# Kernel optimization log

Measured on AMD Instinct MI355X. Metric: run time of the kernel, lower is better.

Reference implementation:

```python
import jax, jax.numpy as jnp
import numpy as np

EPS = 1e-5

def _conv(x, w, b, dil, pad, groups):
    y = jax.lax.conv_general_dilated(
        x, w, window_strides=(1, 1), padding=[(pad, pad), (pad, pad)],
        rhs_dilation=(dil, dil), dimension_numbers=('NCHW', 'OIHW', 'NCHW'),
        feature_group_count=groups)
    return y + b[None, :, None, None]

def setup_inputs() -> dict:
    key = jax.random.key(0)
    ks = jax.random.split(key, 12)
    B, C, H, W = 16, 128, 128, 128
    half = C // 2  # 64
    x = jax.random.normal(ks[0], (B, C, H, W), dtype=jnp.float32)
    # depthwise 3x3 (groups=half) + pointwise 1x1
    dw_w = jax.random.normal(ks[1], (half, 1, 3, 3), dtype=jnp.float32) * 0.1
    dw_b = jax.random.normal(ks[2], (half,), dtype=jnp.float32) * 0.1
    pw_w = jax.random.normal(ks[3], (half, half, 1, 1), dtype=jnp.float32) * (1.0 / np.sqrt(half))
    pw_b = jax.random.normal(ks[4], (half,), dtype=jnp.float32) * 0.1
    # four 1->1 channel 3x3 convs with dilations 1..4 (weights shared across blocks)
    mcc_w = jax.random.normal(ks[5], (4, 1, 1, 3, 3), dtype=jnp.float32) * 0.2
    mcc_b = jax.random.normal(ks[6], (4,), dtype=jnp.float32) * 0.1
    gamma = jnp.ones((C,), dtype=jnp.float32)
    beta = jnp.zeros((C,), dtype=jnp.float32)
    return {"x": x, "dw_w": dw_w, "dw_b": dw_b, "pw_w": pw_w, "pw_b": pw_b,
            "mcc_w": mcc_w, "mcc_b": mcc_b, "gamma": gamma, "beta": beta}

def reference(x, dw_w, dw_b, pw_w, pw_b, mcc_w, mcc_b, gamma, beta):
    B, C, H, W = x.shape
    half = C // 2
    nblk = half // 4
    # split_channel: even channels -> x1, odd channels -> x2
    x1 = x[:, 0::2]
    x2 = x[:, 1::2]
    # branch 1: depthwise 3x3 then pointwise 1x1
    x1 = _conv(x1, dw_w, dw_b, dil=1, pad=1, groups=half)
    x1 = _conv(x1, pw_w, pw_b, dil=1, pad=0, groups=1)
    # branch 2: channel i of x2 goes through dilated conv (i mod 4); vectorize by
    # gathering channels j::4 and running one depthwise conv per dilation.
    ys = []
    for j in range(4):
        d = j + 1
        xj = x2[:, j::4]                       # [B, nblk, H, W]
        wj = jnp.tile(mcc_w[j], (nblk, 1, 1, 1))  # [nblk,1,3,3] shared kernel
        bj = jnp.tile(mcc_b[j], (nblk,))
        ys.append(_conv(xj, wj, bj, dil=d, pad=d, groups=nblk))
    # interleave back: channel 4*b+j <- ys[j][:, b]
    mcc = jnp.stack(ys, axis=2).reshape(B, half, H, W)
    fusion = jnp.concatenate([x1, mcc], axis=1)  # [B, C, H, W]
    # BatchNorm2d (training mode: batch statistics, biased variance) + ReLU
    mean = jnp.mean(fusion, axis=(0, 2, 3), keepdims=True)
    var = jnp.var(fusion, axis=(0, 2, 3), keepdims=True)
    norm = (fusion - mean) * jax.lax.rsqrt(var + EPS)
    out = norm * gamma[None, :, None, None] + beta[None, :, None, None]
    return jax.nn.relu(out)
```

## Files before the change

kernel.cpp:

```cpp
#include <hip/hip_runtime.h>
#include <hip/hip_bf16.h>

#define Bn 16
#define Cn 128
#define Hn 128
#define Wn 128
#define HWn (Hn*Wn)
#define CHWn (Cn*HWn)
#define HALF 64
#define NTOT (Bn*HWn)
#define NSLOT 32
#define NITEM 10240

#define DT_P 76
#define CB_P 136
#define SMEM_BYTES 22528

typedef __attribute__((ext_vector_type(8))) short short8;
typedef __attribute__((ext_vector_type(4))) float floatx4;
typedef float __attribute__((ext_vector_type(4))) f32x4;

__device__ __forceinline__ float4 fma4(float s, float4 v, float4 a) {
  a.x = fmaf(s, v.x, a.x); a.y = fmaf(s, v.y, a.y);
  a.z = fmaf(s, v.z, a.z); a.w = fmaf(s, v.w, a.w);
  return a;
}
__device__ __forceinline__ unsigned short f2bf(float f) {
  union { __hip_bfloat16 h; unsigned short u; } cv;
  cv.h = __float2bfloat16(f); return cv.u;
}
__device__ __forceinline__ float bf2f(unsigned short u) {
  union { unsigned short u; __hip_bfloat16 h; } cv; cv.u = u;
  return __bfloat162float(cv.h);
}
__device__ __forceinline__ unsigned pk2f(float a, float b) {
  return (unsigned)f2bf(a) | ((unsigned)f2bf(b) << 16);
}
__device__ __forceinline__ short8 ld_frag(const unsigned short* p) {
  union { uint2 u[2]; short8 s; } cv;
  cv.u[0] = *(const uint2*)p;
  cv.u[1] = *(const uint2*)(p + 4);
  return cv.s;
}
__device__ __forceinline__ void st_nt4(float* p, float4 v) {
  f32x4 w = {v.x, v.y, v.z, v.w};
  __builtin_nontemporal_store(w, (f32x4*)p);
}

__device__ __forceinline__ float4 row3(float4 acc, float4 B, float wa, float wb,
                                       float wc, int lane31) {
  float xl = __shfl_up(B.w, 1);
  float xr = __shfl_down(B.x, 1);
  if (lane31 == 0)  xl = 0.f;
  if (lane31 == 31) xr = 0.f;
  float4 L = make_float4(xl, B.x, B.y, B.z);
  float4 R = make_float4(B.y, B.z, B.w, xr);
  acc = fma4(wa, L, acc);
  acc = fma4(wb, B, acc);
  acc = fma4(wc, R, acc);
  return acc;
}

template<bool BF16>
__device__ __forceinline__ void dwpw_body(
    const int item, const int t, unsigned char* __restrict__ smem,
    const float* __restrict__ x, const float* __restrict__ pw_w,
    const float* __restrict__ dw_w, const float* __restrict__ dw_b,
    const float* __restrict__ pw_b, float* __restrict__ outf,
    __hip_bfloat16* __restrict__ outh, float* __restrict__ stats)
{
  unsigned short* DtCb = (unsigned short*)smem;
  float* dww  = (float*)(smem + 128*DT_P*2);
  float* sred = dww + 640;

  const int band = item & 7;
  const int ri   = item >> 3;
  const int h = band*16 + (ri & 15);
  const int b = ri >> 4;

  for (int i = t; i < 576; i += 256) {
    int k = i / 9, j = i - k*9;
    dww[j*64 + k] = dw_w[i];
  }
  if (t < 64)  dww[576 + t] = dw_b[t];
  if (t < 128) sred[t] = 0.f;
  __syncthreads();

  {
    const int lane31 = t & 31;
    const int px4 = lane31 << 2;
    const int k0 = t >> 5;
    const float* xb = x + (size_t)b*CHWn + (size_t)h*Wn + px4;
    const bool hasU = (h > 0), hasD = (h < Hn-1);
    const float4 z4 = make_float4(0.f,0.f,0.f,0.f);
    unsigned lo[4];
    #pragma unroll
    for (int i = 0; i < 8; ++i) {
      const int k = k0*8 + i;
      const float* xc = xb + (size_t)(2*k)*HWn;
      float4 r0 = hasU ? *(const float4*)(xc - Wn) : z4;
      float4 r1 = *(const float4*)xc;
      float4 r2 = hasD ? *(const float4*)(xc + Wn) : z4;
      float bk = dww[576 + k];
      float4 a = make_float4(bk, bk, bk, bk);
      a = row3(a, r0, dww[0*64+k], dww[1*64+k], dww[2*64+k], lane31);
      a = row3(a, r1, dww[3*64+k], dww[4*64+k], dww[5*64+k], lane31);
      a = row3(a, r2, dww[6*64+k], dww[7*64+k], dww[8*64+k], lane31);
      float av[4] = {a.x, a.y, a.z, a.w};
      if ((i & 1) == 0) {
        #pragma unroll
        for (int j = 0; j < 4; ++j) lo[j] = f2bf(av[j]);
      } else {
        #pragma unroll
        for (int j = 0; j < 4; ++j) {
          unsigned pk = lo[j] | ((unsigned)f2bf(av[j]) << 16);
          *(unsigned*)&DtCb[(px4+j)*DT_P + k0*8 + (i-1)] = pk;
        }
      }
    }
  }
  __syncthreads();

  const int lane = t & 63;
  const int wv   = t >> 6;
  const int q4   = lane >> 4;
  const int n16  = lane & 15;

  short8 Af[4][2], Bf[2][2];
  #pragma unroll
  for (int ct = 0; ct < 4; ++ct)
    #pragma unroll
    for (int kc = 0; kc < 2; ++kc) {
      const float* wp = pw_w + (ct*16 + n16)*64 + kc*32 + q4*8;
      float4 w0 = *(const float4*)wp;
      float4 w1 = *(const float4*)(wp + 4);
      union { unsigned u[4]; short8 s; } cv;
      cv.u[0] = pk2f(w0.x, w0.y); cv.u[1] = pk2f(w0.z, w0.w);
      cv.u[2] = pk2f(w1.x, w1.y); cv.u[3] = pk2f(w1.z, w1.w);
      Af[ct][kc] = cv.s;
    }
  #pragma unroll
  for (int nt = 0; nt < 2; ++nt)
    #pragma unroll
    for (int kc = 0; kc < 2; ++kc)
      Bf[nt][kc] = ld_frag(&DtCb[(wv*32 + nt*16 + n16)*DT_P + kc*32 + q4*8]);

  floatx4 C[4][2];
  #pragma unroll
  for (int ct = 0; ct < 4; ++ct) {
    float4 bs = *(const float4*)&pw_b[ct*16 + q4*4];
    floatx4 ini = {bs.x, bs.y, bs.z, bs.w};
    C[ct][0] = ini; C[ct][1] = ini;
  }
  #pragma unroll
  for (int kc = 0; kc < 2; ++kc)
    #pragma unroll
    for (int ct = 0; ct < 4; ++ct)
      #pragma unroll
      for (int nt = 0; nt < 2; ++nt)
        C[ct][nt] = __builtin_amdgcn_mfma_f32_16x16x32_bf16(
            Af[ct][kc], Bf[nt][kc], C[ct][nt], 0, 0, 0);

  __syncthreads();

  #pragma unroll
  for (int ct = 0; ct < 4; ++ct) {
    float S[4], Q[4];
    #pragma unroll
    for (int r = 0; r < 4; ++r) {
      float a = C[ct][0][r], c2 = C[ct][1][r];
      S[r] = a + c2;
      Q[r] = a*a + c2*c2;
    }
    #pragma unroll
    for (int off = 1; off < 16; off <<= 1)
      #pragma unroll
      for (int r = 0; r < 4; ++r) {
        S[r] += __shfl_xor(S[r], off);
        Q[r] += __shfl_xor(Q[r], off);
      }
    if (n16 == 0) {
      #pragma unroll
      for (int r = 0; r < 4; ++r) {
        int c = ct*16 + q4*4 + r;
        atomicAdd(&sred[c], S[r]);
        atomicAdd(&sred[64 + c], Q[r]);
      }
    }
  }

  const size_t ob = (size_t)b*CHWn + (size_t)h*Wn;
  if (BF16) {
    #pragma unroll
    for (int ct = 0; ct < 4; ++ct)
      #pragma unroll
      for (int nt = 0; nt < 2; ++nt)
        #pragma unroll
        for (int r = 0; r < 4; ++r) {
          int c  = ct*16 + q4*4 + r;
          int px = wv*32 + nt*16 + n16;
          DtCb[c*CB_P + px] = f2bf(C[ct][nt][r]);
        }
  } else {
    #pragma unroll
    for (int ct = 0; ct < 4; ++ct)
      #pragma unroll
      for (int nt = 0; nt < 2; ++nt)
        #pragma unroll
        for (int r = 0; r < 4; ++r) {
          int c  = ct*16 + q4*4 + r;
          int px = wv*32 + nt*16 + n16;
          outf[ob + (size_t)c*HWn + px] = C[ct][nt][r];
        }
  }
  __syncthreads();

  if (BF16) {
    for (int i = t; i < 1024; i += 256) {
      int c = i >> 4, p8 = (i & 15) << 3;
      uint4 v = *(const uint4*)&DtCb[c*CB_P + p8];
      *(uint4*)(outh + ob + (size_t)c*HWn + p8) = v;
    }
  }

  float* sg = stats + (item & (NSLOT-1))*256;
  if (t < 64)       atomicAdd(&sg[t], sred[t]);
  else if (t < 128) atomicAdd(&sg[64 + t], sred[t]);
}

template<int D> __device__ __forceinline__ float4 shiftL(float4 A, float4 B) {
  if (D == 1) return make_float4(A.w, B.x, B.y, B.z);
  if (D == 2) return make_float4(A.z, A.w, B.x, B.y);
  if (D == 3) return make_float4(A.y, A.z, A.w, B.x);
  return A;
}
template<int D> __device__ __forceinline__ float4 shiftR(float4 B, float4 C) {
  if (D == 1) return make_float4(B.y, B.z, B.w, C.x);
  if (D == 2) return make_float4(B.z, B.w, C.x, C.y);
  if (D == 3) return make_float4(B.w, C.x, C.y, C.z);
  return C;
}

template<bool BF16, int D>
__device__ __forceinline__ void mcc_compute(
    const float* __restrict__ xc, const float* __restrict__ wj, float bj,
    float* __restrict__ outf, __hip_bfloat16* __restrict__ outh,
    float* lds, int t, int h0, float& s, float& q)
{
  const int R = 16 + 2*D;
  for (int idx = t; idx < R*32; idx += 256) {
    int r = idx >> 5, p4 = (idx & 31) << 2;
    int gr = h0 - D + r;
    float4 v = make_float4(0.f,0.f,0.f,0.f);
    if (gr >= 0 && gr < Hn) v = *(const float4*)(xc + gr*Wn + p4);
    *(float4*)&lds[r*128 + p4] = v;
  }
  __syncthreads();
  const int px4 = (t & 31) << 2;
  const int rl  = t >> 5;
  s = 0.f; q = 0.f;
  #pragma unroll
  for (int rr = 0; rr < 2; ++rr) {
    const int row = rl + rr*8;
    float4 acc = make_float4(bj, bj, bj, bj);
    #pragma unroll
    for (int dr = 0; dr < 3; ++dr) {
      const float* lrow = &lds[(row + dr*D)*128];
      float4 B4 = *(const float4*)(lrow + px4);
      float4 A4 = make_float4(0.f,0.f,0.f,0.f);
      float4 C4 = make_float4(0.f,0.f,0.f,0.f);
      if (px4 > 0)   A4 = *(const float4*)(lrow + px4 - 4);
      if (px4 < 124) C4 = *(const float4*)(lrow + px4 + 4);
      acc = fma4(wj[dr*3+0], shiftL<D>(A4, B4), acc);
      acc = fma4(wj[dr*3+1], B4, acc);
      acc = fma4(wj[dr*3+2], shiftR<D>(B4, C4), acc);
    }
    if (BF16) {
      uint2 pk; pk.x = pk2f(acc.x, acc.y); pk.y = pk2f(acc.z, acc.w);
      *(uint2*)(outh + (size_t)(h0+row)*Wn + px4) = pk;
    } else {
      *(float4*)(outf + (size_t)(h0+row)*Wn + px4) = acc;
    }
    s += acc.x + acc.y + acc.z + acc.w;
    q += acc.x*acc.x + acc.y*acc.y + acc.z*acc.z + acc.w*acc.w;
  }
}

template<bool BF16>
__device__ __forceinline__ void mcc_body(
    const int mi, const int t, unsigned char* __restrict__ smem,
    const float* __restrict__ x, const float* __restrict__ mcc_w,
    const float* __restrict__ mcc_b, float* __restrict__ outf,
    __hip_bfloat16* __restrict__ outh, float* __restrict__ stats)
{
  float* lds = (float*)smem;
  float* red = lds + 24*128;

  const int hb = mi & 7;
  const int m  = (mi >> 3) & 63;
  const int b  = mi >> 9;
  const int j  = m & 3;
  const int h0 = hb << 4;

  const float* xc = x + (size_t)b*CHWn + (size_t)(2*m+1)*HWn;
  const size_t oo = (size_t)b*CHWn + (size_t)(HALF+m)*HWn;
  float* of = BF16 ? nullptr : outf + oo;
  __hip_bfloat16* oh = BF16 ? outh + oo : nullptr;
  const float* wj = mcc_w + j*9;
  const float bj = mcc_b[j];

  float s = 0.f, q = 0.f;
  switch (j) {
    case 0:  mcc_compute<BF16,1>(xc, wj, bj, of, oh, lds, t, h0, s, q); break;
    case 1:  mcc_compute<BF16,2>(xc, wj, bj, of, oh, lds, t, h0, s, q); break;
    case 2:  mcc_compute<BF16,3>(xc, wj, bj, of, oh, lds, t, h0, s, q); break;
    default: mcc_compute<BF16,4>(xc, wj, bj, of, oh, lds, t, h0, s, q); break;
  }

  #pragma unroll
  for (int off = 32; off > 0; off >>= 1) {
    s += __shfl_down(s, off);
    q += __shfl_down(q, off);
  }
  const int wvi = t >> 6;
  if ((t & 63) == 0) { red[wvi] = s; red[4+wvi] = q; }
  __syncthreads();
  if (t == 0) {
    float* sg = stats + (mi & (NSLOT-1))*256;
    atomicAdd(&sg[HALF + m],       red[0]+red[1]+red[2]+red[3]);
    atomicAdd(&sg[128 + HALF + m], red[4]+red[5]+red[6]+red[7]);
  }
}

template<bool BF16>
__global__ __launch_bounds__(256, 3) void fused_kernel(
    const float* __restrict__ x, const float* __restrict__ pw_w,
    const float* __restrict__ dw_w, const float* __restrict__ dw_b,
    const float* __restrict__ pw_b, const float* __restrict__ mcc_w,
    const float* __restrict__ mcc_b, float* __restrict__ outf,
    __hip_bfloat16* __restrict__ outh, float* __restrict__ stats)
{
  __shared__ __align__(16) unsigned char smem[SMEM_BYTES];
  const int bid = blockIdx.x;
  const int t = threadIdx.x;
  const int qt = bid / 5;
  if (bid - qt*5 == 0)
    dwpw_body<BF16>(qt, t, smem, x, pw_w, dw_w, dw_b, pw_b, outf, outh, stats);
  else
    mcc_body<BF16>(bid - qt - 1, t, smem, x, mcc_w, mcc_b, outf, outh, stats);
}

__global__ __launch_bounds__(64) void finalize_kernel(
    const float* __restrict__ stats, const float* __restrict__ gamma,
    const float* __restrict__ beta, float* __restrict__ scsh)
{
  const int c = blockIdx.x;
  const int t = threadIdx.x;
  int idx = (t < 32) ? c : (128 + c);
  float v = stats[(t & 31)*256 + idx];
  #pragma unroll
  for (int off = 1; off < 32; off <<= 1) v += __shfl_xor(v, off);
  float S = __shfl(v, 0);
  float Q = __shfl(v, 32);
  if (t == 0) {
    const float n = (float)NTOT;
    float mean = S / n;
    float var  = Q / n - mean*mean;
    float sc = gamma[c] / sqrtf(var + 1e-5f);
    scsh[2*c]   = sc;
    scsh[2*c+1] = beta[c] - mean*sc;
  }
}

__global__ __launch_bounds__(256) void norm_bf_kernel(
    const unsigned short* __restrict__ inh, float* __restrict__ out,
    const float* __restrict__ scsh)
{
  const int blk = blockIdx.x;
  const int plane = blk >> 2;
  const int quarter = blk & 3;
  const int c = plane & 127;
  const float sc = scsh[2*c], sh = scsh[2*c+1];
  const int t = threadIdx.x;

  const uint4* in = (const uint4*)(inh + (size_t)plane*HWn) + quarter*512;
  float* op = out + (size_t)plane*HWn + quarter*4096;
  uint4 p[2];
  #pragma unroll
  for (int i = 0; i < 2; ++i) p[i] = in[t + i*256];
  #pragma unroll
  for (int i = 0; i < 2; ++i) {
    int idx = t + i*256;
    float4 a, bq;
    a.x = fmaxf(fmaf(bf2f(p[i].x & 0xffff), sc, sh), 0.f);
    a.y = fmaxf(fmaf(bf2f(p[i].x >> 16),    sc, sh), 0.f);
    a.z = fmaxf(fmaf(bf2f(p[i].y & 0xffff), sc, sh), 0.f);
    a.w = fmaxf(fmaf(bf2f(p[i].y >> 16),    sc, sh), 0.f);
    bq.x = fmaxf(fmaf(bf2f(p[i].z & 0xffff), sc, sh), 0.f);
    bq.y = fmaxf(fmaf(bf2f(p[i].z >> 16),    sc, sh), 0.f);
    bq.z = fmaxf(fmaf(bf2f(p[i].w & 0xffff), sc, sh), 0.f);
    bq.w = fmaxf(fmaf(bf2f(p[i].w >> 16),    sc, sh), 0.f);
    st_nt4(op + idx*8,     a);
    st_nt4(op + idx*8 + 4, bq);
  }
}

__global__ __launch_bounds__(256) void norm_f32_kernel(float* __restrict__ out,
    const float* __restrict__ scsh)
{
  const int blk = blockIdx.x;
  const int plane = blk >> 2;
  const int quarter = blk & 3;
  const int c = plane & 127;
  const float sc = scsh[2*c], sh = scsh[2*c+1];
  float* op = out + (size_t)plane*HWn + quarter*4096;
  #pragma unroll
  for (int i = 0; i < 4; ++i) {
    int idx = threadIdx.x + i*256;
    float4 v = ((const float4*)op)[idx];
    v.x = fmaxf(fmaf(v.x, sc, sh), 0.f);
    v.y = fmaxf(fmaf(v.y, sc, sh), 0.f);
    v.z = fmaxf(fmaf(v.z, sc, sh), 0.f);
    v.w = fmaxf(fmaf(v.w, sc, sh), 0.f);
    ((float4*)op)[idx] = v;
  }
}

extern "C" void kernel_launch(void* const* d_in, const int* in_sizes, int n_in,
                              void* d_out, int out_size, void* d_ws, size_t ws_size,
                              hipStream_t stream)
{
  (void)in_sizes; (void)n_in; (void)out_size;
  const float* x     = (const float*)d_in[0];
  const float* dw_w  = (const float*)d_in[1];
  const float* dw_b  = (const float*)d_in[2];
  const float* pw_w  = (const float*)d_in[3];
  const float* pw_b  = (const float*)d_in[4];
  const float* mcc_w = (const float*)d_in[5];
  const float* mcc_b = (const float*)d_in[6];
  const float* gamma = (const float*)d_in[7];
  const float* beta  = (const float*)d_in[8];
  float* out   = (float*)d_out;
  float* stats = (float*)d_ws;
  float* scsh  = (float*)((char*)d_ws + 32768);
  __hip_bfloat16* bf = (__hip_bfloat16*)((char*)d_ws + 34816);
  const size_t need = 34816 + (size_t)Bn*CHWn*2;
  const bool useBF = ws_size >= need;

  hipMemsetAsync(d_ws, 0, 32768, stream);
  if (useBF) {
    fused_kernel<true><<<NITEM, 256, 0, stream>>>(x, pw_w, dw_w, dw_b, pw_b,
                                                  mcc_w, mcc_b, nullptr, bf, stats);
    finalize_kernel<<<Cn, 64, 0, stream>>>(stats, gamma, beta, scsh);
    norm_bf_kernel<<<Bn*Cn*4, 256, 0, stream>>>((const unsigned short*)bf, out, scsh);
  } else {
    fused_kernel<false><<<NITEM, 256, 0, stream>>>(x, pw_w, dw_w, dw_b, pw_b,
                                                   mcc_w, mcc_b, out, nullptr, stats);
    finalize_kernel<<<Cn, 64, 0, stream>>>(stats, gamma, beta, scsh);
    norm_f32_kernel<<<Bn*Cn*4, 256, 0, stream>>>(out, scsh);
  }
}
```

Baseline: 315.3 us.

## Enlarge dilated-conv row tiles, hoist depthwise loads, use plain output stores

The dilated-conv work items now cover 32 rows instead of 16, which halves the number of those blocks and cuts the relative halo reload overhead. The fused grid shrinks to match, keeping one depthwise/pointwise block per two dilated-conv blocks. In the depthwise stage, all 24 float4 input loads are issued up front to expose more memory-level parallelism. The final normalize kernel also switches from nontemporal stores to regular stores. The risks are higher register pressure under the 3-blocks-per-CU launch bound and fewer blocks available for load balancing.

```diff
diff --git a/kernel.cpp b/kernel.cpp
--- a/kernel.cpp
+++ b/kernel.cpp
@@ -10,7 +10,7 @@
 #define HALF 64
 #define NTOT (Bn*HWn)
 #define NSLOT 32
-#define NITEM 10240
+#define NBLK 6144
 
 #define DT_P 76
 #define CB_P 136
@@ -18,7 +18,6 @@
 
 typedef __attribute__((ext_vector_type(8))) short short8;
 typedef __attribute__((ext_vector_type(4))) float floatx4;
-typedef float __attribute__((ext_vector_type(4))) f32x4;
 
 __device__ __forceinline__ float4 fma4(float s, float4 v, float4 a) {
   a.x = fmaf(s, v.x, a.x); a.y = fmaf(s, v.y, a.y);
@@ -41,10 +40,6 @@
   cv.u[0] = *(const uint2*)p;
   cv.u[1] = *(const uint2*)(p + 4);
   return cv.s;
-}
-__device__ __forceinline__ void st_nt4(float* p, float4 v) {
-  f32x4 w = {v.x, v.y, v.z, v.w};
-  __builtin_nontemporal_store(w, (f32x4*)p);
 }
 
 __device__ __forceinline__ float4 row3(float4 acc, float4 B, float wa, float wb,
@@ -93,19 +88,25 @@
     const float* xb = x + (size_t)b*CHWn + (size_t)h*Wn + px4;
     const bool hasU = (h > 0), hasD = (h < Hn-1);
     const float4 z4 = make_float4(0.f,0.f,0.f,0.f);
+
+    float4 R0[8], R1[8], R2[8];
+    #pragma unroll
+    for (int i = 0; i < 8; ++i) {
+      const float* xc = xb + (size_t)(2*(k0*8 + i))*HWn;
+      R0[i] = hasU ? *(const float4*)(xc - Wn) : z4;
+      R1[i] = *(const float4*)xc;
+      R2[i] = hasD ? *(const float4*)(xc + Wn) : z4;
+    }
+
     unsigned lo[4];
     #pragma unroll
     for (int i = 0; i < 8; ++i) {
       const int k = k0*8 + i;
-      const float* xc = xb + (size_t)(2*k)*HWn;
-      float4 r0 = hasU ? *(const float4*)(xc - Wn) : z4;
-      float4 r1 = *(const float4*)xc;
-      float4 r2 = hasD ? *(const float4*)(xc + Wn) : z4;
       float bk = dww[576 + k];
       float4 a = make_float4(bk, bk, bk, bk);
-      a = row3(a, r0, dww[0*64+k], dww[1*64+k], dww[2*64+k], lane31);
-      a = row3(a, r1, dww[3*64+k], dww[4*64+k], dww[5*64+k], lane31);
-      a = row3(a, r2, dww[6*64+k], dww[7*64+k], dww[8*64+k], lane31);
+      a = row3(a, R0[i], dww[0*64+k], dww[1*64+k], dww[2*64+k], lane31);
+      a = row3(a, R1[i], dww[3*64+k], dww[4*64+k], dww[5*64+k], lane31);
+      a = row3(a, R2[i], dww[6*64+k], dww[7*64+k], dww[8*64+k], lane31);
       float av[4] = {a.x, a.y, a.z, a.w};
       if ((i & 1) == 0) {
         #pragma unroll
@@ -247,7 +248,7 @@
     float* __restrict__ outf, __hip_bfloat16* __restrict__ outh,
     float* lds, int t, int h0, float& s, float& q)
 {
-  const int R = 16 + 2*D;
+  const int R = 32 + 2*D;
   for (int idx = t; idx < R*32; idx += 256) {
     int r = idx >> 5, p4 = (idx & 31) << 2;
     int gr = h0 - D + r;
@@ -260,7 +261,7 @@
   const int rl  = t >> 5;
   s = 0.f; q = 0.f;
   #pragma unroll
-  for (int rr = 0; rr < 2; ++rr) {
+  for (int rr = 0; rr < 4; ++rr) {
     const int row = rl + rr*8;
     float4 acc = make_float4(bj, bj, bj, bj);
     #pragma unroll
@@ -294,13 +295,13 @@
     __hip_bfloat16* __restrict__ outh, float* __restrict__ stats)
 {
   float* lds = (float*)smem;
-  float* red = lds + 24*128;
-
-  const int hb = mi & 7;
-  const int m  = (mi >> 3) & 63;
-  const int b  = mi >> 9;
+  float* red = (float*)(smem + 40*128*4);
+
+  const int hb = mi & 3;
+  const int m  = (mi >> 2) & 63;
+  const int b  = mi >> 8;
   const int j  = m & 3;
-  const int h0 = hb << 4;
+  const int h0 = hb << 5;
 
   const float* xc = x + (size_t)b*CHWn + (size_t)(2*m+1)*HWn;
   const size_t oo = (size_t)b*CHWn + (size_t)(HALF+m)*HWn;
@@ -343,8 +344,8 @@
   __shared__ __align__(16) unsigned char smem[SMEM_BYTES];
   const int bid = blockIdx.x;
   const int t = threadIdx.x;
-  const int qt = bid / 5;
-  if (bid - qt*5 == 0)
+  const int qt = bid / 3;
+  if (bid - qt*3 == 0)
     dwpw_body<BF16>(qt, t, smem, x, pw_w, dw_w, dw_b, pw_b, outf, outh, stats);
   else
     mcc_body<BF16>(bid - qt - 1, t, smem, x, mcc_w, mcc_b, outf, outh, stats);
@@ -400,8 +401,8 @@
     bq.y = fmaxf(fmaf(bf2f(p[i].z >> 16),    sc, sh), 0.f);
     bq.z = fmaxf(fmaf(bf2f(p[i].w & 0xffff), sc, sh), 0.f);
     bq.w = fmaxf(fmaf(bf2f(p[i].w >> 16),    sc, sh), 0.f);
-    st_nt4(op + idx*8,     a);
-    st_nt4(op + idx*8 + 4, bq);
+    *(float4*)(op + idx*8)     = a;
+    *(float4*)(op + idx*8 + 4) = bq;
   }
 }
 
@@ -449,13 +450,13 @@
 
   hipMemsetAsync(d_ws, 0, 32768, stream);
   if (useBF) {
-    fused_kernel<true><<<NITEM, 256, 0, stream>>>(x, pw_w, dw_w, dw_b, pw_b,
-                                                  mcc_w, mcc_b, nullptr, bf, stats);
+    fused_kernel<true><<<NBLK, 256, 0, stream>>>(x, pw_w, dw_w, dw_b, pw_b,
+                                                 mcc_w, mcc_b, nullptr, bf, stats);
     finalize_kernel<<<Cn, 64, 0, stream>>>(stats, gamma, beta, scsh);
     norm_bf_kernel<<<Bn*Cn*4, 256, 0, stream>>>((const unsigned short*)bf, out, scsh);
   } else {
-    fused_kernel<false><<<NITEM, 256, 0, stream>>>(x, pw_w, dw_w, dw_b, pw_b,
-                                                   mcc_w, mcc_b, out, nullptr, stats);
+    fused_kernel<false><<<NBLK, 256, 0, stream>>>(x, pw_w, dw_w, dw_b, pw_b,
+                                                  mcc_w, mcc_b, out, nullptr, stats);
     finalize_kernel<<<Cn, 64, 0, stream>>>(stats, gamma, beta, scsh);
     norm_f32_kernel<<<Bn*Cn*4, 256, 0, stream>>>(out, scsh);
   }
```

Measured after the change: 321.9 us. +2.1%, slower.

## Merge conv, stats finalize and normalize into one cooperative persistent kernel

Applied to the files above, without the earlier changes.

Replaces the three-kernel sequence (fused conv with stats, finalize, normalize) with a single cooperative persistent kernel that loops over work items and separates the phases with grid-wide syncs. The aim is to remove two kernel launch gaps and tail effects between phases. The cost is a smaller persistent grid limited by occupancy, a grid-stride loop over 10240 items that may balance worse, and the overhead of grid barriers.

```diff
diff --git a/kernel.cpp b/kernel.cpp
--- a/kernel.cpp
+++ b/kernel.cpp
@@ -1,5 +1,8 @@
 #include <hip/hip_runtime.h>
 #include <hip/hip_bf16.h>
+#include <hip/hip_cooperative_groups.h>
+
+namespace cg = cooperative_groups;
 
 #define Bn 16
 #define Cn 128
@@ -332,56 +335,14 @@
   }
 }
 
-template<bool BF16>
-__global__ __launch_bounds__(256, 3) void fused_kernel(
-    const float* __restrict__ x, const float* __restrict__ pw_w,
-    const float* __restrict__ dw_w, const float* __restrict__ dw_b,
-    const float* __restrict__ pw_b, const float* __restrict__ mcc_w,
-    const float* __restrict__ mcc_b, float* __restrict__ outf,
-    __hip_bfloat16* __restrict__ outh, float* __restrict__ stats)
-{
-  __shared__ __align__(16) unsigned char smem[SMEM_BYTES];
-  const int bid = blockIdx.x;
-  const int t = threadIdx.x;
-  const int qt = bid / 5;
-  if (bid - qt*5 == 0)
-    dwpw_body<BF16>(qt, t, smem, x, pw_w, dw_w, dw_b, pw_b, outf, outh, stats);
-  else
-    mcc_body<BF16>(bid - qt - 1, t, smem, x, mcc_w, mcc_b, outf, outh, stats);
-}
-
-__global__ __launch_bounds__(64) void finalize_kernel(
-    const float* __restrict__ stats, const float* __restrict__ gamma,
-    const float* __restrict__ beta, float* __restrict__ scsh)
-{
-  const int c = blockIdx.x;
-  const int t = threadIdx.x;
-  int idx = (t < 32) ? c : (128 + c);
-  float v = stats[(t & 31)*256 + idx];
-  #pragma unroll
-  for (int off = 1; off < 32; off <<= 1) v += __shfl_xor(v, off);
-  float S = __shfl(v, 0);
-  float Q = __shfl(v, 32);
-  if (t == 0) {
-    const float n = (float)NTOT;
-    float mean = S / n;
-    float var  = Q / n - mean*mean;
-    float sc = gamma[c] / sqrtf(var + 1e-5f);
-    scsh[2*c]   = sc;
-    scsh[2*c+1] = beta[c] - mean*sc;
-  }
-}
-
-__global__ __launch_bounds__(256) void norm_bf_kernel(
+__device__ __forceinline__ void norm_quarter(
     const unsigned short* __restrict__ inh, float* __restrict__ out,
-    const float* __restrict__ scsh)
-{
-  const int blk = blockIdx.x;
+    const float* __restrict__ scsh, int blk, int t)
+{
   const int plane = blk >> 2;
   const int quarter = blk & 3;
   const int c = plane & 127;
   const float sc = scsh[2*c], sh = scsh[2*c+1];
-  const int t = threadIdx.x;
 
   const uint4* in = (const uint4*)(inh + (size_t)plane*HWn) + quarter*512;
   float* op = out + (size_t)plane*HWn + quarter*4096;
@@ -403,6 +364,96 @@
     st_nt4(op + idx*8,     a);
     st_nt4(op + idx*8 + 4, bq);
   }
+}
+
+__device__ __forceinline__ void finalize_one(
+    const float* __restrict__ stats, const float* __restrict__ gamma,
+    const float* __restrict__ beta, float* __restrict__ scsh, int c, int t)
+{
+  if (t < 64) {
+    int idx = (t < 32) ? c : (128 + c);
+    float v = stats[(t & 31)*256 + idx];
+    #pragma unroll
+    for (int off = 1; off < 32; off <<= 1) v += __shfl_xor(v, off);
+    float S = __shfl(v, 0);
+    float Q = __shfl(v, 32);
+    if (t == 0) {
+      const float n = (float)NTOT;
+      float mean = S / n;
+      float var  = Q / n - mean*mean;
+      float sc = gamma[c] / sqrtf(var + 1e-5f);
+      scsh[2*c]   = sc;
+      scsh[2*c+1] = beta[c] - mean*sc;
+    }
+  }
+}
+
+__global__ __launch_bounds__(256, 3) void mega_kernel(
+    const float* __restrict__ x, const float* __restrict__ pw_w,
+    const float* __restrict__ dw_w, const float* __restrict__ dw_b,
+    const float* __restrict__ pw_b, const float* __restrict__ mcc_w,
+    const float* __restrict__ mcc_b, const float* __restrict__ gamma,
+    const float* __restrict__ beta, __hip_bfloat16* __restrict__ bf,
+    float* __restrict__ stats, float* __restrict__ scsh,
+    float* __restrict__ out)
+{
+  __shared__ __align__(16) unsigned char smem[SMEM_BYTES];
+  cg::grid_group gg = cg::this_grid();
+  const int t = threadIdx.x;
+  const int G = gridDim.x;
+
+  for (int item = blockIdx.x; item < NITEM; item += G) {
+    __syncthreads();
+    const int q = item / 5;
+    if (item - q*5 == 0)
+      dwpw_body<true>(q, t, smem, x, pw_w, dw_w, dw_b, pw_b,
+                      nullptr, bf, stats);
+    else
+      mcc_body<true>(item - q - 1, t, smem, x, mcc_w, mcc_b,
+                     nullptr, bf, stats);
+  }
+  __threadfence();
+  gg.sync();
+
+  for (int c = blockIdx.x; c < Cn; c += G)
+    finalize_one(stats, gamma, beta, scsh, c, t);
+  __threadfence();
+  gg.sync();
+
+  for (int hp = blockIdx.x; hp < Bn*Cn*4; hp += G)
+    norm_quarter((const unsigned short*)bf, out, scsh, hp, t);
+}
+
+template<bool BF16>
+__global__ __launch_bounds__(256, 3) void fused_kernel(
+    const float* __restrict__ x, const float* __restrict__ pw_w,
+    const float* __restrict__ dw_w, const float* __restrict__ dw_b,
+    const float* __restrict__ pw_b, const float* __restrict__ mcc_w,
+    const float* __restrict__ mcc_b, float* __restrict__ outf,
+    __hip_bfloat16* __restrict__ outh, float* __restrict__ stats)
+{
+  __shared__ __align__(16) unsigned char smem[SMEM_BYTES];
+  const int bid = blockIdx.x;
+  const int t = threadIdx.x;
+  const int qt = bid / 5;
+  if (bid - qt*5 == 0)
+    dwpw_body<BF16>(qt, t, smem, x, pw_w, dw_w, dw_b, pw_b, outf, outh, stats);
+  else
+    mcc_body<BF16>(bid - qt - 1, t, smem, x, mcc_w, mcc_b, outf, outh, stats);
+}
+
+__global__ __launch_bounds__(64) void finalize_kernel(
+    const float* __restrict__ stats, const float* __restrict__ gamma,
+    const float* __restrict__ beta, float* __restrict__ scsh)
+{
+  finalize_one(stats, gamma, beta, scsh, blockIdx.x, threadIdx.x);
+}
+
+__global__ __launch_bounds__(256) void norm_bf_kernel(
+    const unsigned short* __restrict__ inh, float* __restrict__ out,
+    const float* __restrict__ scsh)
+{
+  norm_quarter(inh, out, scsh, blockIdx.x, threadIdx.x);
 }
 
 __global__ __launch_bounds__(256) void norm_f32_kernel(float* __restrict__ out,
@@ -447,8 +498,36 @@
   const size_t need = 34816 + (size_t)Bn*CHWn*2;
   const bool useBF = ws_size >= need;
 
+  static int g_init = 0, g_coop = 0, g_grid = 0;
+  if (!g_init) {
+    int dev = 0; (void)hipGetDevice(&dev);
+    int sup = 0;
+    (void)hipDeviceGetAttribute(&sup, hipDeviceAttributeCooperativeLaunch, dev);
+    hipDeviceProp_t prop;
+    (void)hipGetDeviceProperties(&prop, dev);
+    int nb = 0;
+    (void)hipOccupancyMaxActiveBlocksPerMultiprocessor(&nb, mega_kernel, 256, 0);
+    long G = (long)nb * prop.multiProcessorCount;
+    G = (G / 40) * 40;
+    if (G > 2040) G = 2040;
+    g_grid = (int)G;
+    g_coop = (sup && G >= 40) ? 1 : 0;
+    g_init = 1;
+  }
+
   hipMemsetAsync(d_ws, 0, 32768, stream);
-  if (useBF) {
+  if (useBF && g_coop) {
+    void* args[13];
+    args[0]  = (void*)&x;     args[1]  = (void*)&pw_w;
+    args[2]  = (void*)&dw_w;  args[3]  = (void*)&dw_b;
+    args[4]  = (void*)&pw_b;  args[5]  = (void*)&mcc_w;
+    args[6]  = (void*)&mcc_b; args[7]  = (void*)&gamma;
+    args[8]  = (void*)&beta;  args[9]  = (void*)&bf;
+    args[10] = (void*)&stats; args[11] = (void*)&scsh;
+    args[12] = (void*)&out;
+    (void)hipLaunchCooperativeKernel(mega_kernel, dim3(g_grid), dim3(256),
+                                     args, 0, stream);
+  } else if (useBF) {
     fused_kernel<true><<<NITEM, 256, 0, stream>>>(x, pw_w, dw_w, dw_b, pw_b,
                                                   mcc_w, mcc_b, nullptr, bf, stats);
     finalize_kernel<<<Cn, 64, 0, stream>>>(stats, gamma, beta, scsh);
```

After: 806.6 us. +155.8%, slower.
